# Kernel tuning notes

Hardware: AMD Instinct MI355X
Metric: run time of the kernel (lower is better)

Reference implementation:

```python
import jax, jax.numpy as jnp
import numpy as np

NUM_HEADS = 16
HEAD_DIM = 64


def _rotate_half(x):
    half = x.shape[-1] // 2
    return jnp.concatenate([-x[..., half:], x[..., :half]], axis=-1)


def setup_inputs() -> dict:
    key = jax.random.key(0)
    ks = jax.random.split(key, 7)
    B, S, C = 4, 2048, 1024
    D = HEAD_DIM
    return {
        "hidden_states": jax.random.normal(ks[0], (B, S, C), dtype=jnp.float32),
        "cos": jax.random.uniform(ks[1], (B, S, D), dtype=jnp.float32),
        "sin": jax.random.uniform(ks[2], (B, S, D), dtype=jnp.float32),
        "qkv_w": jax.random.normal(ks[3], (3 * C, C), dtype=jnp.float32) * (C ** -0.5),
        "qkv_b": jax.random.normal(ks[4], (3 * C,), dtype=jnp.float32) * 0.02,
        "proj_w": jax.random.normal(ks[5], (C, C), dtype=jnp.float32) * (C ** -0.5),
        "proj_b": jax.random.normal(ks[6], (C,), dtype=jnp.float32) * 0.02,
    }


def reference(hidden_states, cos, sin, qkv_w, qkv_b, proj_w, proj_b):
    B, S, C = hidden_states.shape
    H, D = NUM_HEADS, HEAD_DIM
    # Fused QKV projection: [B,S,3C] -> [B,S,3,H,D]
    qkv = (hidden_states @ qkv_w.T + qkv_b).reshape(B, S, 3, H, D)
    q, k, v = qkv[:, :, 0], qkv[:, :, 1], qkv[:, :, 2]  # each [B,S,H,D]
    # 2D RoPE in fp32, cos/sin broadcast over heads
    orig_dtype = q.dtype
    cosf = cos[:, :, None, :].astype(jnp.float32)
    sinf = sin[:, :, None, :].astype(jnp.float32)
    qf = q.astype(jnp.float32)
    kf = k.astype(jnp.float32)
    q = (qf * cosf + _rotate_half(qf) * sinf).astype(orig_dtype)
    k = (kf * cosf + _rotate_half(kf) * sinf).astype(orig_dtype)
    # Scaled dot-product attention (non-causal), default scale 1/sqrt(D)
    scale = D ** -0.5
    scores = jnp.einsum("bqhd,bkhd->bhqk", q, k) * scale  # [B,H,S,S]
    probs = jax.nn.softmax(scores, axis=-1)
    attn = jnp.einsum("bhqk,bkhd->bqhd", probs, v).reshape(B, S, C)
    return attn @ proj_w.T + proj_b
```

## Files before the change

### kernel.cpp

```cpp
#include <hip/hip_runtime.h>
#include <hip/hip_bf16.h>


typedef unsigned short u16;
using bf16x8 = __attribute__((ext_vector_type(8))) __bf16;
using f32x4  = __attribute__((ext_vector_type(4))) float;
using f16x4  = __attribute__((ext_vector_type(4))) _Float16;
using f16x2  = __attribute__((ext_vector_type(2))) _Float16;
using fp16v2 = __attribute__((ext_vector_type(2))) __fp16;

#define LDT 80

__device__ __forceinline__ u16 f2bf(float f) {
  union { float f; unsigned u; } un; un.f = f;
  unsigned r = un.u + 0x7FFFu + ((un.u >> 16) & 1u);
  return (u16)(r >> 16);
}

__device__ __forceinline__ f16x2 pk16(float a, float b) {
  union { fp16v2 v; f16x2 f; } u;
  u.v = __builtin_amdgcn_cvt_pkrtz(a, b);
  return u.f;
}

__device__ __forceinline__ void glds16(const void* g, void* l) {
  __builtin_amdgcn_global_load_lds(
      (__attribute__((address_space(1))) void*)(g),
      (__attribute__((address_space(3))) void*)(l), 16, 0, 0);
}

__global__ __launch_bounds__(256) void f2bf_kernel(
    const float* __restrict__ src, u16* __restrict__ dst, int n4)
{
  int i = blockIdx.x * 256 + threadIdx.x;
  if (i < n4) {
    float4 v = ((const float4*)src)[i];
    ushort4 o;
    o.x = f2bf(v.x); o.y = f2bf(v.y); o.z = f2bf(v.z); o.w = f2bf(v.w);
    ((ushort4*)dst)[i] = o;
  }
}

__device__ __forceinline__ void gemm_core_128(
    const u16* __restrict__ A, const u16* __restrict__ Bm, int K,
    int row0, int col0, u16* As, u16* Bs, f32x4 acc[4][4])
{
  const int tid = threadIdx.x;
  const int lane = tid & 63;
  const int w  = tid >> 6;
  const int wm = (w >> 1) << 6;
  const int wn = (w & 1) << 6;
  const int lr = lane & 15;
  const int lq = lane >> 4;
  const int lrow = lane >> 3;
  const int lcol8 = lane & 7;

  for (int k0 = 0; k0 < K; k0 += 64) {
    __syncthreads();
#pragma unroll
    for (int p = 0; p < 4; ++p) {
      int base = w * 32 + p * 8;
      int rr = base + lrow;
      int cc = (lcol8 ^ (rr & 7)) << 3;
      glds16(A  + (size_t)(row0 + rr) * K + k0 + cc, &As[base * 64]);
      glds16(Bm + (size_t)(col0 + rr) * K + k0 + cc, &Bs[base * 64]);
    }
    __syncthreads();
#pragma unroll
    for (int kx = 0; kx < 2; ++kx) {
      bf16x8 af[4], bv[4];
      const int sl = (((kx << 2) + lq) ^ (lr & 7)) << 3;
#pragma unroll
      for (int i = 0; i < 4; ++i) {
        af[i] = *(const bf16x8*)(&As[(wm + i * 16 + lr) * 64 + sl]);
        bv[i] = *(const bf16x8*)(&Bs[(wn + i * 16 + lr) * 64 + sl]);
      }
#pragma unroll
      for (int i = 0; i < 4; ++i)
#pragma unroll
        for (int j = 0; j < 4; ++j)
          acc[i][j] = __builtin_amdgcn_mfma_f32_16x16x32_bf16(af[i], bv[j], acc[i][j], 0, 0, 0);
    }
  }
}

__global__ __launch_bounds__(256) void qkv_gemm_kernel(
    const u16* __restrict__ hs, const u16* __restrict__ wq,
    const float* __restrict__ bias,
    const float* __restrict__ cs, const float* __restrict__ sn,
    u16* __restrict__ Q, u16* __restrict__ K, u16* __restrict__ V)
{
  __shared__ __align__(16) u16 As[128 * 64];
  __shared__ __align__(16) u16 Bs[128 * 64];
  f32x4 acc[4][4];
#pragma unroll
  for (int i = 0; i < 4; ++i)
#pragma unroll
    for (int j = 0; j < 4; ++j) acc[i][j] = (f32x4){0.f, 0.f, 0.f, 0.f};

  const int row0 = blockIdx.y * 128;
  const int col0 = blockIdx.x * 128;
  gemm_core_128(hs, wq, 1024, row0, col0, As, Bs, acc);

  const int lane = threadIdx.x & 63;
  const int w = threadIdx.x >> 6;
  const int lr = lane & 15, lq = lane >> 4;
  const int wm = (w >> 1) << 6, wn = (w & 1) << 6;
  const int ncol = col0 + wn;
  const int wh = ncol >> 10;
  const int h  = (ncol & 1023) >> 6;
  u16* dst = (wh == 0) ? Q : ((wh == 1) ? K : V);
  const float b0 = bias[ncol + lr];
  const float b1 = bias[ncol + 16 + lr];
  const float b2 = bias[ncol + 32 + lr];
  const float b3 = bias[ncol + 48 + lr];

#pragma unroll
  for (int i = 0; i < 4; ++i)
#pragma unroll
    for (int r = 0; r < 4; ++r) {
      int m = row0 + wm + i * 16 + lq * 4 + r;
      float v0 = acc[i][0][r] + b0;
      float v1 = acc[i][1][r] + b1;
      float v2 = acc[i][2][r] + b2;
      float v3 = acc[i][3][r] + b3;
      int b = m >> 11, s = m & 2047;
      size_t off = ((size_t)((b << 4) + h) * 2048 + s) * 64;
      if (wh == 2) {
        union { _Float16 h2; u16 u; } c0, c1, c2, c3;
        c0.h2 = (_Float16)v0; c1.h2 = (_Float16)v1;
        c2.h2 = (_Float16)v2; c3.h2 = (_Float16)v3;
        dst[off + lr]      = c0.u;
        dst[off + 16 + lr] = c1.u;
        dst[off + 32 + lr] = c2.u;
        dst[off + 48 + lr] = c3.u;
      } else {
        size_t cb = (size_t)m << 6;
        float o0 = v0 * cs[cb + lr]      - v2 * sn[cb + lr];
        float o1 = v1 * cs[cb + 16 + lr] - v3 * sn[cb + 16 + lr];
        float o2 = v2 * cs[cb + 32 + lr] + v0 * sn[cb + 32 + lr];
        float o3 = v3 * cs[cb + 48 + lr] + v1 * sn[cb + 48 + lr];
        float sc8 = (wh == 0) ? 0.1803368801f : 1.0f;
        dst[off + lr]      = f2bf(o0 * sc8);
        dst[off + 16 + lr] = f2bf(o1 * sc8);
        dst[off + 32 + lr] = f2bf(o2 * sc8);
        dst[off + 48 + lr] = f2bf(o3 * sc8);
      }
    }
}

__global__ __launch_bounds__(256) void vtrans_kernel(
    const u16* __restrict__ V, u16* __restrict__ Vt)
{
  __shared__ __align__(16) u16 T[64][LDT];
  const int bh = blockIdx.y;
  const int s0 = blockIdx.x * 64;
  const u16* src = V + ((size_t)bh * 2048 + s0) * 64;
  const int r = threadIdx.x >> 2;
  const int c = (threadIdx.x & 3) << 4;
  *(uint4*)(&T[r][c])     = *(const uint4*)(src + r * 64 + c);
  *(uint4*)(&T[r][c + 8]) = *(const uint4*)(src + r * 64 + c + 8);
  __syncthreads();
  alignas(16) u16 tmp[16];
#pragma unroll
  for (int j = 0; j < 16; ++j) tmp[j] = T[c + j][r];
  u16* dst = Vt + ((size_t)bh * 64 + r) * 2048 + s0 + c;
  *(uint4*)(dst)     = *(uint4*)(&tmp[0]);
  *(uint4*)(dst + 8) = *(uint4*)(&tmp[8]);
}

__global__ __launch_bounds__(256, 4) void attn_kernel(
    const u16* __restrict__ Q, const u16* __restrict__ K,
    const u16* __restrict__ Vt, u16* __restrict__ O)
{
  __shared__ __align__(16) u16 Ks[64 * 64];
  __shared__ __align__(16) u16 Vs[64 * 64];
  const int bh = blockIdx.y;
  const int q0 = blockIdx.x << 7;
  const int b = bh >> 4, h = bh & 15;
  const u16* Qh = Q  + (size_t)bh * (2048 * 64);
  const u16* Kh = K  + (size_t)bh * (2048 * 64);
  const u16* Vh = Vt + (size_t)bh * (64 * 2048);
  const int tid = threadIdx.x, lane = tid & 63, w = tid >> 6;
  const int lr = lane & 15, lq = lane >> 4;
  const int lrow = lane >> 3, lcol8 = lane & 7;
  const int wq0 = w * 32;

  bf16x8 qa[2][2];
#pragma unroll
  for (int mi = 0; mi < 2; ++mi)
#pragma unroll
    for (int kx = 0; kx < 2; ++kx)
      qa[mi][kx] = *(const bf16x8*)(Qh + (size_t)(q0 + wq0 + mi * 16 + lr) * 64 + kx * 32 + lq * 8);

  f32x4 acc_o[2][4];
  float lsum[2] = {0.f, 0.f};
#pragma unroll
  for (int mi = 0; mi < 2; ++mi)
#pragma unroll
    for (int td = 0; td < 4; ++td) acc_o[mi][td] = (f32x4){0.f, 0.f, 0.f, 0.f};

  for (int kv0 = 0; kv0 < 2048; kv0 += 64) {
    __syncthreads();
#pragma unroll
    for (int p = 0; p < 2; ++p) {
      int base = w * 16 + p * 8;
      int rr = base + lrow;
      int cc = (lcol8 ^ (rr & 7)) << 3;
      glds16(Kh + (size_t)(kv0 + rr) * 64 + cc, &Ks[base * 64]);
      glds16(Vh + (size_t)rr * 2048 + kv0 + cc, &Vs[base * 64]);
    }
    __syncthreads();

    f32x4 st[4][2];
#pragma unroll
    for (int tj = 0; tj < 4; ++tj)
#pragma unroll
      for (int mi = 0; mi < 2; ++mi) st[tj][mi] = (f32x4){0.f, 0.f, 0.f, 0.f};
#pragma unroll
    for (int kx = 0; kx < 2; ++kx) {
      bf16x8 ka[4];
#pragma unroll
      for (int tj = 0; tj < 4; ++tj) {
        int row = tj * 16 + lr;
        ka[tj] = *(const bf16x8*)(&Ks[row * 64 + ((((kx << 2) + lq) ^ (lr & 7)) << 3)]);
      }
#pragma unroll
      for (int tj = 0; tj < 4; ++tj)
#pragma unroll
        for (int mi = 0; mi < 2; ++mi)
          st[tj][mi] = __builtin_amdgcn_mfma_f32_16x16x32_bf16(ka[tj], qa[mi][kx], st[tj][mi], 0, 0, 0);
    }

    f16x4 pa[2][4];
#pragma unroll
    for (int mi = 0; mi < 2; ++mi)
#pragma unroll
      for (int tj = 0; tj < 4; ++tj) {
        float e0 = __builtin_amdgcn_exp2f(st[tj][mi][0]);
        float e1 = __builtin_amdgcn_exp2f(st[tj][mi][1]);
        float e2 = __builtin_amdgcn_exp2f(st[tj][mi][2]);
        float e3 = __builtin_amdgcn_exp2f(st[tj][mi][3]);
        lsum[mi] += (e0 + e1) + (e2 + e3);
        f16x2 lo = pk16(e0, e1);
        f16x2 hi = pk16(e2, e3);
        f16x4 p4;
        p4[0] = lo[0]; p4[1] = lo[1]; p4[2] = hi[0]; p4[3] = hi[1];
        pa[mi][tj] = p4;
      }

#pragma unroll
    for (int t16 = 0; t16 < 4; ++t16) {
      f16x4 bv[4];
#pragma unroll
      for (int td = 0; td < 4; ++td) {
        int row = td * 16 + lr;
        int qc = (t16 << 1) + (lq >> 1);
        bv[td] = *(const f16x4*)(&Vs[row * 64 + ((qc ^ (lr & 7)) << 3) + ((lq & 1) << 2)]);
      }
#pragma unroll
      for (int td = 0; td < 4; ++td)
#pragma unroll
        for (int mi = 0; mi < 2; ++mi)
          acc_o[mi][td] = __builtin_amdgcn_mfma_f32_16x16x16f16(pa[mi][t16], bv[td], acc_o[mi][td], 0, 0, 0);
    }
  }

#pragma unroll
  for (int mi = 0; mi < 2; ++mi) {
    lsum[mi] += __shfl_xor(lsum[mi], 16, 64);
    lsum[mi] += __shfl_xor(lsum[mi], 32, 64);
  }
#pragma unroll
  for (int mi = 0; mi < 2; ++mi)
#pragma unroll
    for (int r = 0; r < 4; ++r) {
      float inv = 1.f / __shfl(lsum[mi], lq * 4 + r, 64);
      int qq = q0 + wq0 + mi * 16 + lq * 4 + r;
#pragma unroll
      for (int td = 0; td < 4; ++td) {
        int d = td * 16 + lr;
        O[(size_t)(b * 2048 + qq) * 1024 + h * 64 + d] = f2bf(acc_o[mi][td][r] * inv);
      }
    }
}

__global__ __launch_bounds__(256) void proj_gemm_kernel(
    const u16* __restrict__ X, const u16* __restrict__ wp,
    const float* __restrict__ bias, float* __restrict__ out)
{
  __shared__ __align__(16) u16 As[128 * 64];
  __shared__ __align__(16) u16 Bs[128 * 64];
  f32x4 acc[4][4];
#pragma unroll
  for (int i = 0; i < 4; ++i)
#pragma unroll
    for (int j = 0; j < 4; ++j) acc[i][j] = (f32x4){0.f, 0.f, 0.f, 0.f};

  const int row0 = blockIdx.y * 128;
  const int col0 = blockIdx.x * 128;
  gemm_core_128(X, wp, 1024, row0, col0, As, Bs, acc);

  const int lane = threadIdx.x & 63;
  const int w = threadIdx.x >> 6;
  const int wm = (w >> 1) << 6, wn = (w & 1) << 6;
#pragma unroll
  for (int i = 0; i < 4; ++i)
#pragma unroll
    for (int j = 0; j < 4; ++j)
#pragma unroll
      for (int r = 0; r < 4; ++r) {
        int m = row0 + wm + i * 16 + ((lane >> 4) << 2) + r;
        int n = col0 + wn + j * 16 + (lane & 15);
        out[(size_t)m * 1024 + n] = acc[i][j][r] + bias[n];
      }
}

extern "C" void kernel_launch(void* const* d_in, const int* in_sizes, int n_in,
                              void* d_out, int out_size, void* d_ws, size_t ws_size,
                              hipStream_t stream)
{
  const float* hs   = (const float*)d_in[0];
  const float* cs   = (const float*)d_in[1];
  const float* sn   = (const float*)d_in[2];
  const float* qkvw = (const float*)d_in[3];
  const float* qkvb = (const float*)d_in[4];
  const float* pw   = (const float*)d_in[5];
  const float* pb   = (const float*)d_in[6];
  float* out = (float*)d_out;

  const size_t NQ = (size_t)8192 * 1024;
  u16* hsb   = (u16*)d_ws;
  u16* qkvwb = hsb + NQ;
  u16* pwb   = qkvwb + 3145728;
  u16* Qb    = pwb + 1048576;
  u16* Kb    = Qb + NQ;
  u16* Vb    = Kb + NQ;
  u16* Vtb   = Vb + NQ;
  u16* Ob    = hsb;

  f2bf_kernel<<<8192, 256, 0, stream>>>(hs, hsb, (int)(NQ / 4));
  f2bf_kernel<<<3072, 256, 0, stream>>>(qkvw, qkvwb, 3145728 / 4);
  f2bf_kernel<<<1024, 256, 0, stream>>>(pw, pwb, 1048576 / 4);

  qkv_gemm_kernel<<<dim3(24, 64), 256, 0, stream>>>(hsb, qkvwb, qkvb, cs, sn, Qb, Kb, Vb);
  vtrans_kernel<<<dim3(32, 64), 256, 0, stream>>>(Vb, Vtb);
  attn_kernel<<<dim3(16, 64), 256, 0, stream>>>(Qb, Kb, Vtb, Ob);
  proj_gemm_kernel<<<dim3(8, 64), 256, 0, stream>>>(Ob, pwb, pb, out);
}
```

Baseline: 309.4 us.

## Double-buffer K/V tiles in attention and pre-pack RoPE cos/sin table

The attention kernel now keeps two LDS buffers for K and V. It prefetches the next KV tile with async global-to-LDS loads while computing on the current one, which drops one barrier per iteration and overlaps load latency with MFMA work. Separately, a new kernel packs cos/sin into a bf16 interleaved table so the QKV epilogue does one 16-byte load per row instead of eight scattered fp32 loads. This costs twice the LDS in attention, which may affect the 4-blocks occupancy target, and bf16 rounding of cos/sin adds precision loss. There is also a concern that no wait or barrier follows the prefetch before the next tile is read, since only one __syncthreads per iteration remains.

```diff
diff --git a/kernel.cpp b/kernel.cpp
--- a/kernel.cpp
+++ b/kernel.cpp
@@ -16,6 +16,10 @@
   unsigned r = un.u + 0x7FFFu + ((un.u >> 16) & 1u);
   return (u16)(r >> 16);
 }
+__device__ __forceinline__ float bf2f(u16 b) {
+  union { unsigned u; float f; } un; un.u = ((unsigned)b) << 16;
+  return un.f;
+}
 
 __device__ __forceinline__ f16x2 pk16(float a, float b) {
   union { fp16v2 v; f16x2 f; } u;
@@ -39,6 +43,22 @@
     o.x = f2bf(v.x); o.y = f2bf(v.y); o.z = f2bf(v.z); o.w = f2bf(v.w);
     ((ushort4*)dst)[i] = o;
   }
+}
+
+__global__ __launch_bounds__(256) void rope_table_kernel(
+    const float* __restrict__ cs, const float* __restrict__ sn,
+    u16* __restrict__ RT)
+{
+  int t = blockIdx.x * 256 + threadIdx.x;
+  int lr = t & 15, m = t >> 4;
+  const float* c = cs + (size_t)m * 64;
+  const float* s = sn + (size_t)m * 64;
+  alignas(16) u16 o[8];
+  o[0] = f2bf(c[lr]); o[1] = f2bf(c[lr + 16]);
+  o[2] = f2bf(c[lr + 32]); o[3] = f2bf(c[lr + 48]);
+  o[4] = f2bf(s[lr]); o[5] = f2bf(s[lr + 16]);
+  o[6] = f2bf(s[lr + 32]); o[7] = f2bf(s[lr + 48]);
+  *(uint4*)(RT + (size_t)t * 8) = *(const uint4*)o;
 }
 
 __device__ __forceinline__ void gemm_core_128(
@@ -86,8 +106,7 @@
 
 __global__ __launch_bounds__(256) void qkv_gemm_kernel(
     const u16* __restrict__ hs, const u16* __restrict__ wq,
-    const float* __restrict__ bias,
-    const float* __restrict__ cs, const float* __restrict__ sn,
+    const float* __restrict__ bias, const u16* __restrict__ RT,
     u16* __restrict__ Q, u16* __restrict__ K, u16* __restrict__ V)
 {
   __shared__ __align__(16) u16 As[128 * 64];
@@ -135,11 +154,12 @@
         dst[off + 32 + lr] = c2.u;
         dst[off + 48 + lr] = c3.u;
       } else {
-        size_t cb = (size_t)m << 6;
-        float o0 = v0 * cs[cb + lr]      - v2 * sn[cb + lr];
-        float o1 = v1 * cs[cb + 16 + lr] - v3 * sn[cb + 16 + lr];
-        float o2 = v2 * cs[cb + 32 + lr] + v0 * sn[cb + 32 + lr];
-        float o3 = v3 * cs[cb + 48 + lr] + v1 * sn[cb + 48 + lr];
+        alignas(16) u16 rv[8];
+        *(uint4*)rv = *(const uint4*)(RT + ((size_t)m * 16 + lr) * 8);
+        float o0 = v0 * bf2f(rv[0]) - v2 * bf2f(rv[4]);
+        float o1 = v1 * bf2f(rv[1]) - v3 * bf2f(rv[5]);
+        float o2 = v2 * bf2f(rv[2]) + v0 * bf2f(rv[6]);
+        float o3 = v3 * bf2f(rv[3]) + v1 * bf2f(rv[7]);
         float sc8 = (wh == 0) ? 0.1803368801f : 1.0f;
         dst[off + lr]      = f2bf(o0 * sc8);
         dst[off + 16 + lr] = f2bf(o1 * sc8);
@@ -169,12 +189,26 @@
   *(uint4*)(dst + 8) = *(uint4*)(&tmp[8]);
 }
 
+__device__ __forceinline__ void attn_stage(
+    const u16* __restrict__ Kh, const u16* __restrict__ Vh, int kv0,
+    u16* KsB, u16* VsB, int w, int lrow, int lcol8)
+{
+#pragma unroll
+  for (int p = 0; p < 2; ++p) {
+    int base = w * 16 + p * 8;
+    int rr = base + lrow;
+    int cc = (lcol8 ^ (rr & 7)) << 3;
+    glds16(Kh + (size_t)(kv0 + rr) * 64 + cc, KsB + base * 64);
+    glds16(Vh + (size_t)rr * 2048 + kv0 + cc, VsB + base * 64);
+  }
+}
+
 __global__ __launch_bounds__(256, 4) void attn_kernel(
     const u16* __restrict__ Q, const u16* __restrict__ K,
     const u16* __restrict__ Vt, u16* __restrict__ O)
 {
-  __shared__ __align__(16) u16 Ks[64 * 64];
-  __shared__ __align__(16) u16 Vs[64 * 64];
+  __shared__ __align__(16) u16 Ks[2][64 * 64];
+  __shared__ __align__(16) u16 Vs[2][64 * 64];
   const int bh = blockIdx.y;
   const int q0 = blockIdx.x << 7;
   const int b = bh >> 4, h = bh & 15;
@@ -186,6 +220,8 @@
   const int lrow = lane >> 3, lcol8 = lane & 7;
   const int wq0 = w * 32;
 
+  attn_stage(Kh, Vh, 0, Ks[0], Vs[0], w, lrow, lcol8);
+
   bf16x8 qa[2][2];
 #pragma unroll
   for (int mi = 0; mi < 2; ++mi)
@@ -200,17 +236,13 @@
 #pragma unroll
     for (int td = 0; td < 4; ++td) acc_o[mi][td] = (f32x4){0.f, 0.f, 0.f, 0.f};
 
-  for (int kv0 = 0; kv0 < 2048; kv0 += 64) {
+  for (int it = 0; it < 32; ++it) {
+    const int cur = it & 1;
     __syncthreads();
-#pragma unroll
-    for (int p = 0; p < 2; ++p) {
-      int base = w * 16 + p * 8;
-      int rr = base + lrow;
-      int cc = (lcol8 ^ (rr & 7)) << 3;
-      glds16(Kh + (size_t)(kv0 + rr) * 64 + cc, &Ks[base * 64]);
-      glds16(Vh + (size_t)rr * 2048 + kv0 + cc, &Vs[base * 64]);
-    }
-    __syncthreads();
+    if (it + 1 < 32)
+      attn_stage(Kh, Vh, (it + 1) << 6, Ks[cur ^ 1], Vs[cur ^ 1], w, lrow, lcol8);
+    const u16* Kc = Ks[cur];
+    const u16* Vc = Vs[cur];
 
     f32x4 st[4][2];
 #pragma unroll
@@ -223,7 +255,7 @@
 #pragma unroll
       for (int tj = 0; tj < 4; ++tj) {
         int row = tj * 16 + lr;
-        ka[tj] = *(const bf16x8*)(&Ks[row * 64 + ((((kx << 2) + lq) ^ (lr & 7)) << 3)]);
+        ka[tj] = *(const bf16x8*)(&Kc[row * 64 + ((((kx << 2) + lq) ^ (lr & 7)) << 3)]);
       }
 #pragma unroll
       for (int tj = 0; tj < 4; ++tj)
@@ -256,7 +288,7 @@
       for (int td = 0; td < 4; ++td) {
         int row = td * 16 + lr;
         int qc = (t16 << 1) + (lq >> 1);
-        bv[td] = *(const f16x4*)(&Vs[row * 64 + ((qc ^ (lr & 7)) << 3) + ((lq & 1) << 2)]);
+        bv[td] = *(const f16x4*)(&Vc[row * 64 + ((qc ^ (lr & 7)) << 3) + ((lq & 1) << 2)]);
       }
 #pragma unroll
       for (int td = 0; td < 4; ++td)
@@ -337,13 +369,15 @@
   u16* Kb    = Qb + NQ;
   u16* Vb    = Kb + NQ;
   u16* Vtb   = Vb + NQ;
+  u16* RT    = Vtb + NQ;
   u16* Ob    = hsb;
 
   f2bf_kernel<<<8192, 256, 0, stream>>>(hs, hsb, (int)(NQ / 4));
   f2bf_kernel<<<3072, 256, 0, stream>>>(qkvw, qkvwb, 3145728 / 4);
   f2bf_kernel<<<1024, 256, 0, stream>>>(pw, pwb, 1048576 / 4);
-
-  qkv_gemm_kernel<<<dim3(24, 64), 256, 0, stream>>>(hsb, qkvwb, qkvb, cs, sn, Qb, Kb, Vb);
+  rope_table_kernel<<<512, 256, 0, stream>>>(cs, sn, RT);
+
+  qkv_gemm_kernel<<<dim3(24, 64), 256, 0, stream>>>(hsb, qkvwb, qkvb, RT, Qb, Kb, Vb);
   vtrans_kernel<<<dim3(32, 64), 256, 0, stream>>>(Vb, Vtb);
   attn_kernel<<<dim3(16, 64), 256, 0, stream>>>(Qb, Kb, Vtb, Ob);
   proj_gemm_kernel<<<dim3(8, 64), 256, 0, stream>>>(Ob, pwb, pb, out);
```

Measured after the change: 304.7 us. No clear change (-1.5%).
